# Performance work log

Hardware: AMD Instinct MI355X
Metric: run time of the kernel (lower is better)

## Reference

```python
import jax, jax.numpy as jnp
import numpy as np

N, E, F_IN, H, G, K = 50000, 800000, 64, 200, 256, 3


def setup_inputs() -> dict:
    key = jax.random.key(0)
    ks = jax.random.split(key, 12)
    x = jax.random.normal(ks[0], (N, F_IN), jnp.float32)
    edge_index = jax.random.randint(ks[1], (2, E), 0, N, dtype=jnp.int64)
    batch = jnp.sort(jax.random.randint(ks[2], (N,), 0, G, dtype=jnp.int64))
    lmax = 1.5 + jax.random.uniform(ks[3], (G,), jnp.float32)  # per-graph lambda_max

    def lin(k, i, o):
        return (jax.random.normal(k, (K, i, o), jnp.float32) / np.sqrt(i)).astype(jnp.float32)

    return dict(
        x=x, edge_index=edge_index, batch=batch, lmax=lmax,
        W1=lin(ks[4], F_IN, H), b1=jnp.zeros((H,), jnp.float32),
        W2=lin(ks[5], H, H),    b2=jnp.zeros((H,), jnp.float32),
        W3=lin(ks[6], H, H),    b3=jnp.zeros((H,), jnp.float32),
        W4=lin(ks[7], H, H),    b4=jnp.zeros((H,), jnp.float32),
        fc_w=(jax.random.normal(ks[8], (2 * H, 2), jnp.float32) / np.sqrt(2 * H)).astype(jnp.float32),
        fc_b=jnp.zeros((2,), jnp.float32),
    )


def reference(x, edge_index, batch, lmax, W1, b1, W2, b2, W3, b3, W4, b4, fc_w, fc_b):
    n = x.shape[0]
    g = lmax.shape[0]
    src, dst = edge_index[0], edge_index[1]

    # PyG ChebConv sym normalization: L_hat = 2/lambda_max * (I - D^-1/2 A D^-1/2) - I
    deg = jax.ops.segment_sum(jnp.ones(src.shape[0], x.dtype), src, num_segments=n)
    dis = jnp.where(deg > 0, jnp.maximum(deg, 1.0) ** -0.5, 0.0)  # deg^{-1/2}, inf -> 0
    scale = 2.0 / lmax                                            # [G]
    w = -dis[src] * dis[dst] * scale[batch[src]]                  # off-diagonal edge weights [E]
    diag = scale[batch] - 1.0                                     # diagonal of L_hat, [N]

    def prop(h):  # L_hat @ h via sparse scatter
        return jax.ops.segment_sum(w[:, None] * h[src], dst, num_segments=n) + diag[:, None] * h

    def cheb(h, W, b):  # K=3 Chebyshev recurrence
        Tx0 = h
        Tx1 = prop(h)
        Tx2 = 2.0 * prop(Tx1) - Tx0
        return Tx0 @ W[0] + Tx1 @ W[1] + Tx2 @ W[2] + b

    h = jax.nn.relu(cheb(x, W1, b1))
    h = jax.nn.relu(cheb(h, W2, b2))
    h = jax.nn.relu(cheb(h, W3, b3))
    h = jax.nn.relu(cheb(h, W4, b4))

    cnt = jax.ops.segment_sum(jnp.ones(n, h.dtype), batch, num_segments=g)
    pooled_mean = jax.ops.segment_sum(h, batch, num_segments=g) / jnp.maximum(cnt, 1.0)[:, None]
    pooled_max = jax.ops.segment_max(h, batch, num_segments=g)
    z = jnp.concatenate([pooled_mean, pooled_max], axis=1) @ fc_w + fc_b
    return jax.nn.log_softmax(z, axis=1)
```

## Files before the change

### kernel.cpp

```cpp
#include <hip/hip_runtime.h>
#include <math.h>

#define NN 50000
#define MP 50048
#define NE 800000
#define FIN 64
#define HD 200
#define NG 256
#define SCAN_B 256
#define KPAD 224
#define NT 13
#define HB 12544
#define PER_B 3125

typedef _Float16 h16;
typedef __attribute__((ext_vector_type(8))) _Float16 half8;
typedef __attribute__((ext_vector_type(4))) float float4v;
typedef unsigned long long u64;

__global__ __launch_bounds__(256) void k_hist(const int* __restrict__ src,
                                              const int* __restrict__ dst,
                                              unsigned* __restrict__ pSrc,
                                              unsigned* __restrict__ pDst, int E) {
    __shared__ unsigned h[HB];
    int tid = threadIdx.x;
    int isDst = blockIdx.x >> 8;
    int b = blockIdx.x & 255;
    const int* idx = isDst ? dst : src;
    unsigned* partial = isDst ? pDst : pSrc;
    int e0 = b * PER_B;
    int v[13];
#pragma unroll
    for (int j = 0; j < 13; ++j) {
        int o = j * 256 + tid;
        v[j] = (o < PER_B) ? idx[e0 + o] : -1;
    }
#pragma unroll
    for (int pass = 0; pass < 2; ++pass) {
        for (int t = tid; t < HB; t += 256) h[t] = 0;
        __syncthreads();
        int lo = pass * (2 * HB);
#pragma unroll
        for (int j = 0; j < 13; ++j) {
            int vv = v[j] - lo;
            if (vv >= 0 && vv < 2 * HB)
                atomicAdd(&h[vv >> 1], (vv & 1) ? 0x10000u : 1u);
        }
        __syncthreads();
        unsigned* pb = partial + ((size_t)pass * 256 + b) * HB;
        for (int t = tid; t < HB; t += 256) pb[t] = h[t];
        __syncthreads();
    }
}

__global__ void k_hredscan(const unsigned* __restrict__ pSrc, unsigned* __restrict__ pDst,
                           int* __restrict__ degi, int* __restrict__ cntd, int n) {
    int i = blockIdx.x * blockDim.x + threadIdx.x;
    if (i < 2 * HB) {
        int pass = i / HB, p = i - pass * HB;
        const unsigned* pb = pSrc + (size_t)pass * 256 * HB + p;
        unsigned s = 0;
        for (int b = 0; b < 256; ++b) s += pb[(size_t)b * HB];
        int n0 = pass * 2 * HB + 2 * p;
        if (n0 < n)     degi[n0]     = (int)(s & 0xffffu);
        if (n0 + 1 < n) degi[n0 + 1] = (int)(s >> 16);
    } else if (i < 4 * HB) {
        int j = i - 2 * HB;
        int pass = j / HB, p = j - pass * HB;
        unsigned* pb = pDst + (size_t)pass * 256 * HB + p;
        unsigned run = 0;
        for (int b = 0; b < 256; ++b) {
            unsigned c = pb[(size_t)b * HB];
            pb[(size_t)b * HB] = run;
            run += c;
        }
        int n0 = pass * 2 * HB + 2 * p;
        if (n0 < n)     cntd[n0]     = (int)(run & 0xffffu);
        if (n0 + 1 < n) cntd[n0 + 1] = (int)(run >> 16);
    }
}

__global__ void k_prep(const int* __restrict__ degi, const int* __restrict__ batch,
                       const float* __restrict__ lmax, float* __restrict__ dis,
                       float* __restrict__ qs, float* __restrict__ diag,
                       int* __restrict__ gstart, int n, int gN) {
    int b = blockIdx.x;
    if (b < gN) {
        int i = b * 256 + threadIdx.x;
        if (i < n) {
            int d = degi[i];
            float di = (d > 0) ? (1.0f / sqrtf((float)d)) : 0.0f;
            float sc = 2.0f / lmax[batch[i]];
            dis[i] = di;
            qs[i] = -di * sc;
            diag[i] = sc - 1.0f;
        }
    } else {
        int g = (b - gN) * 256 + threadIdx.x;
        if (g > NG) return;
        if (g == NG) { gstart[NG] = n; return; }
        int lo = 0, hi = n;
        while (lo < hi) {
            int mid = (lo + hi) >> 1;
            if (batch[mid] < g) lo = mid + 1; else hi = mid;
        }
        gstart[g] = lo;
    }
}

__global__ void k_scan1(const int* __restrict__ cnt, int* __restrict__ excl,
                        int* __restrict__ bsum, int n) {
    __shared__ int sh[SCAN_B];
    int tid = threadIdx.x;
    int i = blockIdx.x * SCAN_B + tid;
    int v = (i < n) ? cnt[i] : 0;
    sh[tid] = v;
    __syncthreads();
    for (int off = 1; off < SCAN_B; off <<= 1) {
        int t = (tid >= off) ? sh[tid - off] : 0;
        __syncthreads();
        sh[tid] += t;
        __syncthreads();
    }
    if (i < n) excl[i] = sh[tid] - v;
    if (tid == SCAN_B - 1) bsum[blockIdx.x] = sh[tid];
}

__global__ void k_scan2(int* __restrict__ bsum, int nb) {
    __shared__ int sh[SCAN_B];
    int tid = threadIdx.x;
    int v = (tid < nb) ? bsum[tid] : 0;
    sh[tid] = v;
    __syncthreads();
    for (int off = 1; off < SCAN_B; off <<= 1) {
        int t = (tid >= off) ? sh[tid - off] : 0;
        __syncthreads();
        sh[tid] += t;
        __syncthreads();
    }
    if (tid < nb) bsum[tid] = sh[tid] - v;
}

__global__ __launch_bounds__(256) void k_fillcsr2(
    const int* __restrict__ src, const int* __restrict__ dst,
    const float* __restrict__ qs, const float* __restrict__ dis,
    const int* __restrict__ excl, const int* __restrict__ bsum,
    const unsigned* __restrict__ hpart, u64* __restrict__ csr, int E) {
    __shared__ unsigned lrank[HB];
    int tid = threadIdx.x;
    int e0 = blockIdx.x * PER_B;
    int vs[13], vd[13];
#pragma unroll
    for (int j = 0; j < 13; ++j) {
        int o = j * 256 + tid;
        vs[j] = (o < PER_B) ? src[e0 + o] : -1;
        vd[j] = (o < PER_B) ? dst[e0 + o] : -1;
    }
#pragma unroll
    for (int pass = 0; pass < 2; ++pass) {
        for (int t = tid; t < HB; t += 256) lrank[t] = 0;
        __syncthreads();
        int lo = pass * (2 * HB);
        const unsigned* base = hpart + ((size_t)pass * 256 + blockIdx.x) * HB;
#pragma unroll
        for (int j = 0; j < 13; ++j) {
            int vv = vd[j] - lo;
            if (vv >= 0 && vv < 2 * HB) {
                unsigned old = atomicAdd(&lrank[vv >> 1], (vv & 1) ? 0x10000u : 1u);
                unsigned rank = (vv & 1) ? (old >> 16) : (old & 0xffffu);
                unsigned bs = base[vv >> 1];
                unsigned bb = (vv & 1) ? (bs >> 16) : (bs & 0xffffu);
                int s = vs[j], d = vd[j];
                int pos = excl[d] + bsum[d >> 8] + (int)bb + (int)rank;
                float w = qs[s] * dis[d];
                csr[pos] = (unsigned)s | ((u64)__float_as_uint(w) << 32);
            }
        }
        __syncthreads();
    }
}

__global__ void k_wprep(const float* __restrict__ W1, const float* __restrict__ W2,
                        const float* __restrict__ W3, const float* __restrict__ W4,
                        h16* __restrict__ wt0, h16* __restrict__ wt1,
                        h16* __restrict__ wt2, h16* __restrict__ wt3,
                        const float* __restrict__ x, h16* __restrict__ x16) {
    const int T0 = 3 * 2 * 208 * 32, T = 3 * 7 * 208 * 32;
    const int TW = T0 + 3 * T;
    int idx = blockIdx.x * blockDim.x + threadIdx.x;
    if (idx >= TW) {
        int i = idx - TW;
        if (i < NN * FIN) x16[i] = (h16)x[i];
        return;
    }
    const float* W; h16* o; int fin, ksteps, li;
    if (idx < T0) { W = W1; o = wt0; fin = FIN; ksteps = 2; li = idx; }
    else {
        int r = idx - T0; int l = r / T;
        li = r - l * T; fin = HD; ksteps = 7;
        W = (l == 0) ? W2 : ((l == 1) ? W3 : W4);
        o = (l == 0) ? wt1 : ((l == 1) ? wt2 : wt3);
    }
    int kk = li & 31;
    int r2 = li >> 5;
    int nn = r2 % 208;
    int r3 = r2 / 208;
    int ks = r3 % ksteps;
    int seg = r3 / ksteps;
    int k = ks * 32 + kk;
    o[li] = (nn < HD && k < fin) ? (h16)W[((size_t)seg * fin + k) * HD + nn] : (h16)0.f;
}

__global__ __launch_bounds__(256) void k_gather(
    const int* __restrict__ excl, const int* __restrict__ bsum,
    const int* __restrict__ rowcnt,
    const u64* __restrict__ csr, const float* __restrict__ diag,
    const h16* __restrict__ hin16, const h16* __restrict__ h016,
    h16* __restrict__ hout16, int s16, int lsh, int n, int mode) {
    int per = 256 >> lsh;
    int i = blockIdx.x * per + (threadIdx.x >> lsh);
    if (i >= n) return;
    int lane = threadIdx.x & ((1 << lsh) - 1);
    int c0 = lane * 4;
    if (c0 >= s16) return;
    int start = excl[i] + bsum[i >> 8];
    int cnt = rowcnt[i];
    float g0 = 0.f, g1 = 0.f, g2 = 0.f, g3 = 0.f;
    union U { uint2 u; h16 h[4]; };
    const u64* cp = csr + start;
    int k = 0;
    for (; k + 7 < cnt; k += 8) {
        u64 e[8];
#pragma unroll
        for (int j = 0; j < 8; ++j) e[j] = cp[k + j];
        U p[8];
#pragma unroll
        for (int j = 0; j < 8; ++j)
            p[j].u = *(const uint2*)(hin16 + (size_t)(unsigned)(e[j] & 0xffffffffu) * s16 + c0);
#pragma unroll
        for (int j = 0; j < 8; ++j) {
            float w = __uint_as_float((unsigned)(e[j] >> 32));
            g0 += w * (float)p[j].h[0];
            g1 += w * (float)p[j].h[1];
            g2 += w * (float)p[j].h[2];
            g3 += w * (float)p[j].h[3];
        }
    }
    for (; k + 1 < cnt; k += 2) {
        u64 e0 = cp[k], e1 = cp[k + 1];
        U p0, p1;
        p0.u = *(const uint2*)(hin16 + (size_t)(unsigned)(e0 & 0xffffffffu) * s16 + c0);
        p1.u = *(const uint2*)(hin16 + (size_t)(unsigned)(e1 & 0xffffffffu) * s16 + c0);
        float w0 = __uint_as_float((unsigned)(e0 >> 32));
        float w1 = __uint_as_float((unsigned)(e1 >> 32));
        g0 += w0 * (float)p0.h[0] + w1 * (float)p1.h[0];
        g1 += w0 * (float)p0.h[1] + w1 * (float)p1.h[1];
        g2 += w0 * (float)p0.h[2] + w1 * (float)p1.h[2];
        g3 += w0 * (float)p0.h[3] + w1 * (float)p1.h[3];
    }
    if (k < cnt) {
        u64 e0 = cp[k];
        U p0;
        p0.u = *(const uint2*)(hin16 + (size_t)(unsigned)(e0 & 0xffffffffu) * s16 + c0);
        float w0 = __uint_as_float((unsigned)(e0 >> 32));
        g0 += w0 * (float)p0.h[0];
        g1 += w0 * (float)p0.h[1];
        g2 += w0 * (float)p0.h[2];
        g3 += w0 * (float)p0.h[3];
    }
    float dg = diag[i];
    U hs; hs.u = *(const uint2*)(hin16 + (size_t)i * s16 + c0);
    float v0 = g0 + dg * (float)hs.h[0];
    float v1 = g1 + dg * (float)hs.h[1];
    float v2 = g2 + dg * (float)hs.h[2];
    float v3 = g3 + dg * (float)hs.h[3];
    if (mode == 1) {
        U h0; h0.u = *(const uint2*)(h016 + (size_t)i * s16 + c0);
        v0 = 2.f * v0 - (float)h0.h[0];
        v1 = 2.f * v1 - (float)h0.h[1];
        v2 = 2.f * v2 - (float)h0.h[2];
        v3 = 2.f * v3 - (float)h0.h[3];
    }
    U o;
    o.h[0] = (h16)v0; o.h[1] = (h16)v1; o.h[2] = (h16)v2; o.h[3] = (h16)v3;
    *(uint2*)(hout16 + (size_t)i * s16 + c0) = o.u;
}

__global__ __launch_bounds__(256) void k_gemm16(
    const h16* __restrict__ A0, const h16* __restrict__ A1, const h16* __restrict__ A2,
    int strideA, int ksteps,
    const h16* __restrict__ Wt, const float* __restrict__ bias,
    h16* __restrict__ out16, int n) {
    int tid = threadIdx.x;
    int wave = tid >> 6, lane = tid & 63;
    int nq = lane & 15, quad = lane >> 4;
    int row0 = (blockIdx.x * 4 + wave) * 32;
    const h16* Aseg[3] = {A0, A1, A2};

    float4v acc[2][NT];
#pragma unroll
    for (int r = 0; r < 2; r++)
#pragma unroll
        for (int t = 0; t < NT; t++) acc[r][t] = (float4v)0.f;

    for (int seg = 0; seg < 3; ++seg) {
        const h16* Ab = Aseg[seg] + (size_t)(row0 + nq) * strideA + quad * 8;
        const h16* Bb = Wt + (size_t)seg * ksteps * 208 * 32 + (size_t)nq * 32 + quad * 8;
        for (int ks = 0; ks < ksteps; ++ks) {
            half8 af0 = *(const half8*)(Ab + ks * 32);
            half8 af1 = *(const half8*)(Ab + 16 * strideA + ks * 32);
            const h16* Bk = Bb + (size_t)ks * 208 * 32;
#pragma unroll
            for (int t = 0; t < NT; ++t) {
                half8 bf = *(const half8*)(Bk + t * 16 * 32);
                acc[0][t] = __builtin_amdgcn_mfma_f32_16x16x32_f16(af0, bf, acc[0][t], 0, 0, 0);
                acc[1][t] = __builtin_amdgcn_mfma_f32_16x16x32_f16(af1, bf, acc[1][t], 0, 0, 0);
            }
        }
    }
#pragma unroll
    for (int r = 0; r < 2; ++r) {
        int rowb = row0 + r * 16 + quad * 4;
#pragma unroll
        for (int t = 0; t < NT; ++t) {
            int col = t * 16 + nq;
            if (col >= HD) continue;
            float bj = bias[col];
#pragma unroll
            for (int g = 0; g < 4; ++g) {
                int row = rowb + g;
                if (row < n)
                    out16[(size_t)row * KPAD + col] = (h16)fmaxf(acc[r][t][g] + bj, 0.0f);
            }
        }
    }
}

__global__ __launch_bounds__(256) void k_pool_fc(
    const h16* __restrict__ Hf, const int* __restrict__ gstart,
    const float* __restrict__ fcw, const float* __restrict__ fcb,
    float* __restrict__ out) {
    __shared__ float red[8];
    int g = blockIdx.x;
    int j = threadIdx.x;
    int i0 = gstart[g], i1 = gstart[g + 1];
    float s0 = 0.f, s1 = 0.f, s2 = 0.f, s3 = 0.f, mx = 0.f;
    if (j < HD) {
        int i = i0;
        for (; i + 3 < i1; i += 4) {
            float v0 = (float)Hf[(size_t)i * KPAD + j];
            float v1 = (float)Hf[(size_t)(i + 1) * KPAD + j];
            float v2 = (float)Hf[(size_t)(i + 2) * KPAD + j];
            float v3 = (float)Hf[(size_t)(i + 3) * KPAD + j];
            s0 += v0; s1 += v1; s2 += v2; s3 += v3;
            mx = fmaxf(mx, fmaxf(fmaxf(v0, v1), fmaxf(v2, v3)));
        }
        for (; i < i1; ++i) {
            float v = (float)Hf[(size_t)i * KPAD + j];
            s0 += v; mx = fmaxf(mx, v);
        }
    }
    float cntf = (float)(i1 - i0);
    float mean = (s0 + s1 + s2 + s3) / fmaxf(cntf, 1.f);
    float p0 = 0.f, p1 = 0.f;
    if (j < HD) {
        p0 = mean * fcw[2 * j]     + mx * fcw[2 * (HD + j)];
        p1 = mean * fcw[2 * j + 1] + mx * fcw[2 * (HD + j) + 1];
    }
#pragma unroll
    for (int o = 32; o > 0; o >>= 1) {
        p0 += __shfl_down(p0, o);
        p1 += __shfl_down(p1, o);
    }
    int wave = j >> 6, lane = j & 63;
    if (lane == 0) { red[wave * 2] = p0; red[wave * 2 + 1] = p1; }
    __syncthreads();
    if (j == 0) {
        float z0 = red[0] + red[2] + red[4] + red[6] + fcb[0];
        float z1 = red[1] + red[3] + red[5] + red[7] + fcb[1];
        float m = fmaxf(z0, z1);
        float lse = m + logf(expf(z0 - m) + expf(z1 - m));
        out[g * 2 + 0] = z0 - lse;
        out[g * 2 + 1] = z1 - lse;
    }
}

extern "C" void kernel_launch(void* const* d_in, const int* in_sizes, int n_in,
                              void* d_out, int out_size, void* d_ws, size_t ws_size,
                              hipStream_t stream) {
    const float* x     = (const float*)d_in[0];
    const int*   edge  = (const int*)d_in[1];
    const int*   batch = (const int*)d_in[2];
    const float* lmax  = (const float*)d_in[3];
    const float* W1 = (const float*)d_in[4];  const float* b1 = (const float*)d_in[5];
    const float* W2 = (const float*)d_in[6];  const float* b2 = (const float*)d_in[7];
    const float* W3 = (const float*)d_in[8];  const float* b3 = (const float*)d_in[9];
    const float* W4 = (const float*)d_in[10]; const float* b4 = (const float*)d_in[11];
    const float* fcw = (const float*)d_in[12]; const float* fcb = (const float*)d_in[13];
    float* out = (float*)d_out;

    const int n = NN, E = NE;
    const int* src = edge;
    const int* dst = edge + E;

    float* ws = (float*)d_ws;
    size_t off = 0;
    auto alloc = [&](size_t nfloats) { float* p = ws + off; off += (nfloats + 3) & ~(size_t)3; return p; };
    int*   degi   = (int*)alloc(NN);
    float* dis    = alloc(NN);
    float* qs     = alloc(NN);
    float* diag   = alloc(NN);
    int*   cntd   = (int*)alloc(NN);
    int*   excl   = (int*)alloc(NN);
    int*   bsum   = (int*)alloc(SCAN_B);
    u64*   csr    = (u64*)alloc((size_t)NE * 2);
    int*   gstart = (int*)alloc(NG + 1);
    unsigned* pSrc = (unsigned*)alloc((size_t)2 * 256 * HB);
    unsigned* pDst = (unsigned*)alloc((size_t)2 * 256 * HB);
    h16*   x16    = (h16*)alloc((size_t)MP * FIN / 2);
    h16*   hi0    = (h16*)alloc((size_t)MP * KPAD / 2);
    h16*   hi1    = (h16*)alloc((size_t)MP * KPAD / 2);
    h16*   hi2    = (h16*)alloc((size_t)MP * KPAD / 2);
    const int WSZ0 = 3 * 2 * 208 * 32;
    const int WSZ  = 3 * 7 * 208 * 32;
    h16* wt0 = (h16*)alloc(WSZ0 / 2);
    h16* wt1 = (h16*)alloc(WSZ / 2);
    h16* wt2 = (h16*)alloc(WSZ / 2);
    h16* wt3 = (h16*)alloc(WSZ / 2);

    dim3 blk(256);
    int gN = (n + 255) / 256;
    int gScan = (n + SCAN_B - 1) / SCAN_B;
    int gGemm = MP / 128;
    int gWp = (WSZ0 + 3 * WSZ + NN * FIN + 255) / 256;

    k_wprep<<<gWp, blk, 0, stream>>>(W1, W2, W3, W4, wt0, wt1, wt2, wt3, x, x16);
    k_hist<<<512, blk, 0, stream>>>(src, dst, pSrc, pDst, E);
    k_hredscan<<<(4 * HB + 255) / 256, blk, 0, stream>>>(pSrc, pDst, degi, cntd, n);
    k_prep<<<gN + 2, blk, 0, stream>>>(degi, batch, lmax, dis, qs, diag, gstart, n, gN);
    k_scan1<<<gScan, blk, 0, stream>>>(cntd, excl, bsum, n);
    k_scan2<<<1, blk, 0, stream>>>(bsum, gScan);
    k_fillcsr2<<<256, blk, 0, stream>>>(src, dst, qs, dis, excl, bsum, pDst, csr, E);

    const h16* wt[4] = {wt0, wt1, wt2, wt3};
    const float* bl[4] = {b1, b2, b3, b4};
    for (int l = 0; l < 4; l++) {
        int s16 = (l == 0) ? FIN : KPAD;
        int lsh = (l == 0) ? 4 : 6;
        int per = 256 >> lsh;
        int gGat = (n + per - 1) / per;
        int ksteps = (l == 0) ? 2 : 7;
        const h16* a0 = (l == 0) ? x16 : hi0;
        k_gather<<<gGat, blk, 0, stream>>>(excl, bsum, cntd, csr, diag, a0, a0, hi1, s16, lsh, n, 0);
        k_gather<<<gGat, blk, 0, stream>>>(excl, bsum, cntd, csr, diag, hi1, a0, hi2, s16, lsh, n, 1);
        k_gemm16<<<gGemm, blk, 0, stream>>>(a0, hi1, hi2, s16, ksteps, wt[l], bl[l],
                                            (l < 3) ? hi0 : hi1, n);
    }

    k_pool_fc<<<NG, blk, 0, stream>>>(hi1, gstart, fcw, fcb, out);
}
```

Measured before the change: 781.1 us.

## Fold Chebyshev recurrence into weights and split gather by column groups

The weight prep now folds the Tx2 = 2*L*Tx1 - Tx0 recurrence into the weights: W0-W2, W1, 2*W2. The second gather therefore becomes a plain propagation and no longer reads h0 or runs the combine step. The gather kernel is also restructured so each block handles 32 nodes times one column group of 28 or 32 features with 8 lanes per node. This spreads a node's columns across blocks to improve cache locality of the gathered rows. In exchange the CSR row metadata is re-read once per column group, and fp16 precision behaves slightly differently because the weights are combined before conversion.

```diff
diff --git a/kernel.cpp b/kernel.cpp
--- a/kernel.cpp
+++ b/kernel.cpp
@@ -208,21 +208,29 @@
     int ks = r3 % ksteps;
     int seg = r3 / ksteps;
     int k = ks * 32 + kk;
-    o[li] = (nn < HD && k < fin) ? (h16)W[((size_t)seg * fin + k) * HD + nn] : (h16)0.f;
+    float val = 0.f;
+    if (nn < HD && k < fin) {
+        size_t base = (size_t)k * HD + nn;
+        size_t segsz = (size_t)fin * HD;
+        if (seg == 0)      val = W[base] - W[2 * segsz + base];
+        else if (seg == 1) val = W[segsz + base];
+        else               val = 2.f * W[2 * segsz + base];
+    }
+    o[li] = (h16)val;
 }
 
 __global__ __launch_bounds__(256) void k_gather(
     const int* __restrict__ excl, const int* __restrict__ bsum,
     const int* __restrict__ rowcnt,
     const u64* __restrict__ csr, const float* __restrict__ diag,
-    const h16* __restrict__ hin16, const h16* __restrict__ h016,
-    h16* __restrict__ hout16, int s16, int lsh, int n, int mode) {
-    int per = 256 >> lsh;
-    int i = blockIdx.x * per + (threadIdx.x >> lsh);
+    const h16* __restrict__ hin16, h16* __restrict__ hout16,
+    int s16, int n, int ncg, int cw) {
+    int g = blockIdx.x % ncg;
+    int i = (blockIdx.x / ncg) * 32 + (threadIdx.x >> 3);
     if (i >= n) return;
-    int lane = threadIdx.x & ((1 << lsh) - 1);
-    int c0 = lane * 4;
-    if (c0 >= s16) return;
+    int lane = threadIdx.x & 7;
+    if (lane * 4 >= cw) return;
+    int c0 = g * cw + lane * 4;
     int start = excl[i] + bsum[i >> 8];
     int cnt = rowcnt[i];
     float g0 = 0.f, g1 = 0.f, g2 = 0.f, g3 = 0.f;
@@ -270,19 +278,11 @@
     }
     float dg = diag[i];
     U hs; hs.u = *(const uint2*)(hin16 + (size_t)i * s16 + c0);
-    float v0 = g0 + dg * (float)hs.h[0];
-    float v1 = g1 + dg * (float)hs.h[1];
-    float v2 = g2 + dg * (float)hs.h[2];
-    float v3 = g3 + dg * (float)hs.h[3];
-    if (mode == 1) {
-        U h0; h0.u = *(const uint2*)(h016 + (size_t)i * s16 + c0);
-        v0 = 2.f * v0 - (float)h0.h[0];
-        v1 = 2.f * v1 - (float)h0.h[1];
-        v2 = 2.f * v2 - (float)h0.h[2];
-        v3 = 2.f * v3 - (float)h0.h[3];
-    }
     U o;
-    o.h[0] = (h16)v0; o.h[1] = (h16)v1; o.h[2] = (h16)v2; o.h[3] = (h16)v3;
+    o.h[0] = (h16)(g0 + dg * (float)hs.h[0]);
+    o.h[1] = (h16)(g1 + dg * (float)hs.h[1]);
+    o.h[2] = (h16)(g2 + dg * (float)hs.h[2]);
+    o.h[3] = (h16)(g3 + dg * (float)hs.h[3]);
     *(uint2*)(hout16 + (size_t)i * s16 + c0) = o.u;
 }
 
@@ -444,15 +444,16 @@
 
     const h16* wt[4] = {wt0, wt1, wt2, wt3};
     const float* bl[4] = {b1, b2, b3, b4};
+    int nodeBlks = (n + 31) / 32;
     for (int l = 0; l < 4; l++) {
         int s16 = (l == 0) ? FIN : KPAD;
-        int lsh = (l == 0) ? 4 : 6;
-        int per = 256 >> lsh;
-        int gGat = (n + per - 1) / per;
+        int ncg = (l == 0) ? 2 : 8;
+        int cw  = (l == 0) ? 32 : 28;
+        int gGat = ncg * nodeBlks;
         int ksteps = (l == 0) ? 2 : 7;
         const h16* a0 = (l == 0) ? x16 : hi0;
-        k_gather<<<gGat, blk, 0, stream>>>(excl, bsum, cntd, csr, diag, a0, a0, hi1, s16, lsh, n, 0);
-        k_gather<<<gGat, blk, 0, stream>>>(excl, bsum, cntd, csr, diag, hi1, a0, hi2, s16, lsh, n, 1);
+        k_gather<<<gGat, blk, 0, stream>>>(excl, bsum, cntd, csr, diag, a0, hi1, s16, n, ncg, cw);
+        k_gather<<<gGat, blk, 0, stream>>>(excl, bsum, cntd, csr, diag, hi1, hi2, s16, n, ncg, cw);
         k_gemm16<<<gGemm, blk, 0, stream>>>(a0, hi1, hi2, s16, ksteps, wt[l], bl[l],
                                             (l < 3) ? hi0 : hi1, n);
     }
```

Measured after the change: 1.234 ms. 58.0% more time.
